# Kernel tuning notes

Measured on AMD Instinct MI355X. Metric: run time of the kernel, lower is better.

## Reference

```python
import jax, jax.numpy as jnp
import numpy as np

VOCAB, INPUT, HIDDEN = 50000, 512, 1024
BATCH, MAX_LEN = 64, 256


def setup_inputs() -> dict:
    key = jax.random.key(0)
    ks = jax.random.split(key, 16)
    s = 0.02
    return {
        "last_output": jax.random.randint(ks[0], (BATCH,), 0, VOCAB),
        "last_hidden": jax.random.normal(ks[1], (BATCH, HIDDEN), jnp.float32),
        "encoder_outputs": jax.random.normal(ks[2], (MAX_LEN, BATCH, HIDDEN), jnp.float32),
        # embedding table (padding_idx=0 just means row 0 is a pad row; math is a plain gather)
        "embedding": jax.random.uniform(ks[3], (VOCAB, INPUT), jnp.float32, -0.25, 0.25),
        # concat attention: Linear(2H -> H) and v [H]
        "attn_W": jax.random.normal(ks[4], (HIDDEN, 2 * HIDDEN), jnp.float32) * s,
        "attn_b": jnp.zeros((HIDDEN,), jnp.float32),
        "v": jax.random.normal(ks[5], (HIDDEN,), jnp.float32) * s,
        # GRU (single layer): input size = INPUT + HIDDEN, gate order r,z,n (torch order)
        "W_ih": jax.random.normal(ks[6], (3 * HIDDEN, INPUT + HIDDEN), jnp.float32) * s,
        "W_hh": jax.random.uniform(ks[7], (3 * HIDDEN, HIDDEN), jnp.float32, -0.01, 0.01),
        "b_ih": jnp.zeros((3 * HIDDEN,), jnp.float32),
        "b_hh": jnp.zeros((3 * HIDDEN,), jnp.float32),
        # output projection Linear(2H -> vocab)
        "out_W": jax.random.normal(ks[8], (VOCAB, 2 * HIDDEN), jnp.float32) * s,
        "out_b": jnp.zeros((VOCAB,), jnp.float32),
    }


def reference(last_output, last_hidden, encoder_outputs, embedding,
              attn_W, attn_b, v, W_ih, W_hh, b_ih, b_hh, out_W, out_b):
    T, B, H = encoder_outputs.shape
    # --- embedding lookup: [B, INPUT]
    emb = embedding[last_output]

    # --- concat (Bahdanau-style, no tanh in original) attention, vectorized over T
    hid = jnp.broadcast_to(last_hidden[None], (T, B, H))
    cat = jnp.concatenate([hid, encoder_outputs], axis=-1)          # [T,B,2H]
    energy = jnp.einsum('tbk,hk->tbh', cat, attn_W) + attn_b        # [T,B,H]
    scores = jnp.einsum('tbh,h->bt', energy, v)                     # [B,T]
    attn = jax.nn.softmax(scores, axis=1)                           # [B,T]

    # --- context: [B,H]
    context = jnp.einsum('bt,tbh->bh', attn, encoder_outputs)

    # --- single GRU step (torch gate order r,z,n)
    x = jnp.concatenate([emb, context], axis=-1)                    # [B, INPUT+H]
    gi = x @ W_ih.T + b_ih                                          # [B,3H]
    gh = last_hidden @ W_hh.T + b_hh                                # [B,3H]
    i_r, i_z, i_n = jnp.split(gi, 3, axis=-1)
    h_r, h_z, h_n = jnp.split(gh, 3, axis=-1)
    r = jax.nn.sigmoid(i_r + h_r)
    z = jax.nn.sigmoid(i_z + h_z)
    n = jnp.tanh(i_n + r * h_n)
    h_new = (1.0 - z) * n + z * last_hidden                         # [B,H]

    # --- output projection + log_softmax over vocab
    logits = jnp.concatenate([h_new, context], axis=-1) @ out_W.T + out_b
    logp = jax.nn.log_softmax(logits, axis=-1)                      # [B,VOCAB]
    return logp, h_new
```

## Files before the change

kernel.cpp:

```cpp
#include <hip/hip_runtime.h>
#include <cstddef>

#define VOCAB  50000
#define INPUT  512
#define HIDDEN 1024
#define BATCH  64
#define MAXLEN 256
#define NBLK   782

typedef float  f32x4 __attribute__((ext_vector_type(4)));
typedef __bf16 bf16x8 __attribute__((ext_vector_type(8)));

__device__ __forceinline__ bf16x8 cvt8(float4 a, float4 b) {
    bf16x8 r;
    r[0] = (__bf16)a.x; r[1] = (__bf16)a.y; r[2] = (__bf16)a.z; r[3] = (__bf16)a.w;
    r[4] = (__bf16)b.x; r[5] = (__bf16)b.y; r[6] = (__bf16)b.z; r[7] = (__bf16)b.w;
    return r;
}

__global__ void k_u2_part(const float* __restrict__ attn_W, const float* __restrict__ v,
                          float* __restrict__ u2p) {
    int bid = blockIdx.x, tid = threadIdx.x;
    int hq = bid >> 4, kc = bid & 15;
    int kl = tid & 63, hg = tid >> 6;
    int k = kc * 64 + kl;
    float acc = 0.f;
    int h0 = hq * 256 + hg * 64;
#pragma unroll 8
    for (int h = h0; h < h0 + 64; ++h)
        acc += v[h] * attn_W[(size_t)h * (2 * HIDDEN) + HIDDEN + k];
    __shared__ float red[4][64];
    red[hg][kl] = acc;
    __syncthreads();
    if (tid < 64)
        u2p[hq * 1024 + kc * 64 + tid] =
            red[0][tid] + red[1][tid] + red[2][tid] + red[3][tid];
}

__global__ __launch_bounds__(256) void k_att(const float* __restrict__ enc,
                                             const float* __restrict__ u2p,
                                             float* __restrict__ mpart,
                                             float* __restrict__ lpart,
                                             float* __restrict__ ctxp) {
    int bid = blockIdx.x, tid = threadIdx.x;
    int b = bid >> 2, tq = bid & 3, t0 = tq * 64;
    __shared__ float u2s[1024];
    __shared__ float s_lds[64];
    __shared__ float p_lds[64];
    for (int i = tid; i < 1024; i += 256)
        u2s[i] = u2p[i] + u2p[1024 + i] + u2p[2048 + i] + u2p[3072 + i];
    __syncthreads();
    int w = tid >> 6, lane = tid & 63;
#pragma unroll 2
    for (int it = 0; it < 16; ++it) {
        int t = t0 + w * 16 + it;
        const float* row = enc + ((size_t)t * BATCH + b) * HIDDEN;
        float acc = 0.f;
#pragma unroll
        for (int i = 0; i < 4; ++i) {
            float4 e = *(const float4*)(row + lane * 4 + i * 256);
            float4 u = *(const float4*)(&u2s[lane * 4 + i * 256]);
            acc += e.x * u.x + e.y * u.y + e.z * u.z + e.w * u.w;
        }
#pragma unroll
        for (int off = 32; off; off >>= 1) acc += __shfl_down(acc, off, 64);
        if (lane == 0) s_lds[w * 16 + it] = acc;
    }
    __syncthreads();
    float m = -INFINITY;
#pragma unroll 8
    for (int t = 0; t < 64; ++t) m = fmaxf(m, s_lds[t]);
    if (tid < 64) p_lds[tid] = expf(s_lds[tid] - m);
    __syncthreads();
    float l = 0.f;
#pragma unroll 8
    for (int t = 0; t < 64; ++t) l += p_lds[t];
    float4 acc = {0.f, 0.f, 0.f, 0.f};
    const float* ebase = enc + ((size_t)t0 * BATCH + b) * HIDDEN + tid * 4;
#pragma unroll 4
    for (int t = 0; t < 64; ++t) {
        float p = p_lds[t];
        float4 e = *(const float4*)(ebase + (size_t)t * (BATCH * HIDDEN));
        acc.x += p * e.x; acc.y += p * e.y; acc.z += p * e.z; acc.w += p * e.w;
    }
    int o = b * 4 + tq;
    *(float4*)(ctxp + (size_t)o * 1024 + tid * 4) = acc;
    if (tid == 0) { mpart[o] = m; lpart[o] = l; }
}

__global__ void k_att_comb(const float* __restrict__ mpart, const float* __restrict__ lpart,
                           const float* __restrict__ ctxp,
                           const int* __restrict__ last_output,
                           const float* __restrict__ embedding,
                           const float* __restrict__ hid,
                           __bf16* __restrict__ x_bf, __bf16* __restrict__ hid_bf,
                           __bf16* __restrict__ y_bf) {
    int b = blockIdx.x >> 2, hc = blockIdx.x & 3, tid = threadIdx.x;
    float m0 = mpart[b * 4 + 0], m1 = mpart[b * 4 + 1];
    float m2 = mpart[b * 4 + 2], m3 = mpart[b * 4 + 3];
    float M = fmaxf(fmaxf(m0, m1), fmaxf(m2, m3));
    float w0 = expf(m0 - M), w1 = expf(m1 - M), w2 = expf(m2 - M), w3 = expf(m3 - M);
    float denom = lpart[b * 4 + 0] * w0 + lpart[b * 4 + 1] * w1 +
                  lpart[b * 4 + 2] * w2 + lpart[b * 4 + 3] * w3;
    float inv = 1.f / denom;
    int h = hc * 256 + tid;
    const float* cp = ctxp + (size_t)b * 4096 + h;
    float c = (w0 * cp[0] + w1 * cp[1024] + w2 * cp[2048] + w3 * cp[3072]) * inv;
    x_bf[b * 1536 + INPUT + h]  = (__bf16)c;
    y_bf[b * 2048 + HIDDEN + h] = (__bf16)c;
    if (hc < 2)
        x_bf[b * 1536 + hc * 256 + tid] =
            (__bf16)embedding[(size_t)last_output[b] * INPUT + hc * 256 + tid];
    hid_bf[b * HIDDEN + hc * 256 + tid] = (__bf16)hid[b * HIDDEN + hc * 256 + tid];
}

__device__ __forceinline__ void gemm_tile(const float* __restrict__ W,
                                          const float* __restrict__ bias,
                                          const __bf16* __restrict__ A,
                                          float* __restrict__ out,
                                          int N, int K, int jt, int tid) {
    int wid = tid >> 6, lane = tid & 63;
    int j  = jt * 16 + (lane & 15);
    int kg = (lane >> 4) * 8;
    int kchunk = K >> 2;
    int kbeg = wid * kchunk, kend = kbeg + kchunk;
    const float*  wrow = W + (size_t)j * K;
    const __bf16* arow = A + (size_t)(lane & 15) * K;
    f32x4 acc[4] = {};
    for (int k0 = kbeg; k0 < kend; k0 += 32) {
        int kk = k0 + kg;
        float4 w0 = *(const float4*)(wrow + kk);
        float4 w1 = *(const float4*)(wrow + kk + 4);
        bf16x8 bw = cvt8(w0, w1);
#pragma unroll
        for (int mt = 0; mt < 4; ++mt) {
            bf16x8 av = *(const bf16x8*)(arow + (size_t)mt * 16 * K + kk);
            acc[mt] = __builtin_amdgcn_mfma_f32_16x16x32_bf16(av, bw, acc[mt], 0, 0, 0);
        }
    }
    __shared__ float lds[4][1024];
#pragma unroll
    for (int mt = 0; mt < 4; ++mt)
#pragma unroll
        for (int r = 0; r < 4; ++r) {
            int m = mt * 16 + (lane >> 4) * 4 + r;
            lds[wid][m * 16 + (lane & 15)] = acc[mt][r];
        }
    __syncthreads();
#pragma unroll
    for (int o = tid; o < 1024; o += 256) {
        float s = lds[0][o] + lds[1][o] + lds[2][o] + lds[3][o];
        int m = o >> 4, jl = o & 15;
        out[(size_t)m * N + jt * 16 + jl] = s + bias[jt * 16 + jl];
    }
}

__global__ __launch_bounds__(256) void k_gemm_gru(const float* __restrict__ W_ih,
                                                  const float* __restrict__ b_ih,
                                                  const __bf16* __restrict__ x_bf,
                                                  float* __restrict__ Gi,
                                                  const float* __restrict__ W_hh,
                                                  const float* __restrict__ b_hh,
                                                  const __bf16* __restrict__ hid_bf,
                                                  float* __restrict__ Gh) {
    int bid = blockIdx.x, tid = threadIdx.x;
    if (bid < 192) gemm_tile(W_ih, b_ih, x_bf,  Gi, 3072, 1536, bid,       tid);
    else           gemm_tile(W_hh, b_hh, hid_bf, Gh, 3072, 1024, bid - 192, tid);
}

__global__ void k_combine(const float* __restrict__ Gi, const float* __restrict__ Gh,
                          const float* __restrict__ hid, float* __restrict__ hnew_out,
                          __bf16* __restrict__ y_bf) {
    int idx = blockIdx.x * 256 + threadIdx.x;
    int b = idx >> 10, h = idx & 1023;
    const float* gi = Gi + (size_t)b * 3072;
    const float* gh = Gh + (size_t)b * 3072;
    float r  = 1.f / (1.f + expf(-(gi[h] + gh[h])));
    float z  = 1.f / (1.f + expf(-(gi[1024 + h] + gh[1024 + h])));
    float n  = tanhf(gi[2048 + h] + r * gh[2048 + h]);
    float hp = hid[b * HIDDEN + h];
    float hn = (1.f - z) * n + z * hp;
    hnew_out[b * HIDDEN + h] = hn;
    y_bf[b * 2048 + h] = (__bf16)hn;
}

__global__ __launch_bounds__(256) void k_gemv(const float* __restrict__ W,
                                              const float* __restrict__ bias,
                                              const __bf16* __restrict__ A,
                                              float* __restrict__ out,
                                              float* __restrict__ mw,
                                              float* __restrict__ sw) {
    int bid = blockIdx.x, tid = threadIdx.x;
    int wid = tid >> 6, lane = tid & 63;
    int kg = (lane >> 4) * 8;
    int kbeg = wid * 512;
    int ntiles = (bid == NBLK - 1) ? 1 : 4;
    int j0 = bid * 64 + (lane & 15);
    const float* wrow0 = W + (size_t)min(j0,      VOCAB - 1) * 2048;
    const float* wrow1 = W + (size_t)min(j0 + 16, VOCAB - 1) * 2048;
    const float* wrow2 = W + (size_t)min(j0 + 32, VOCAB - 1) * 2048;
    const float* wrow3 = W + (size_t)min(j0 + 48, VOCAB - 1) * 2048;
    const __bf16* arow = A + (size_t)(lane & 15) * 2048;
    f32x4 acc[4][4] = {};
    for (int k0 = kbeg; k0 < kbeg + 512; k0 += 32) {
        int kk = k0 + kg;
        bf16x8 bw0 = cvt8(*(const float4*)(wrow0 + kk), *(const float4*)(wrow0 + kk + 4));
        bf16x8 bw1 = cvt8(*(const float4*)(wrow1 + kk), *(const float4*)(wrow1 + kk + 4));
        bf16x8 bw2 = cvt8(*(const float4*)(wrow2 + kk), *(const float4*)(wrow2 + kk + 4));
        bf16x8 bw3 = cvt8(*(const float4*)(wrow3 + kk), *(const float4*)(wrow3 + kk + 4));
#pragma unroll
        for (int mt = 0; mt < 4; ++mt) {
            bf16x8 av = *(const bf16x8*)(arow + (size_t)mt * 16 * 2048 + kk);
            acc[0][mt] = __builtin_amdgcn_mfma_f32_16x16x32_bf16(av, bw0, acc[0][mt], 0, 0, 0);
            acc[1][mt] = __builtin_amdgcn_mfma_f32_16x16x32_bf16(av, bw1, acc[1][mt], 0, 0, 0);
            acc[2][mt] = __builtin_amdgcn_mfma_f32_16x16x32_bf16(av, bw2, acc[2][mt], 0, 0, 0);
            acc[3][mt] = __builtin_amdgcn_mfma_f32_16x16x32_bf16(av, bw3, acc[3][mt], 0, 0, 0);
        }
    }
    __shared__ float lds[4][1024];
    float Mreg = -INFINITY, Sreg = 0.f;
    for (int u = 0; u < ntiles; ++u) {
        if (u) __syncthreads();
#pragma unroll
        for (int mt = 0; mt < 4; ++mt)
#pragma unroll
            for (int r = 0; r < 4; ++r) {
                int m = mt * 16 + (lane >> 4) * 4 + r;
                lds[wid][m * 16 + (lane & 15)] = acc[u][mt][r];
            }
        __syncthreads();
#pragma unroll
        for (int o = tid; o < 1024; o += 256) {
            float s = lds[0][o] + lds[1][o] + lds[2][o] + lds[3][o];
            int m = o >> 4, jl = o & 15;
            int jj = bid * 64 + u * 16 + jl;
            s += bias[jj];
            out[(size_t)m * VOCAB + jj] = s;
            lds[0][o] = s;
        }
        __syncthreads();
        if (tid < 64) {
            float mx = -INFINITY;
#pragma unroll
            for (int jl = 0; jl < 16; ++jl) mx = fmaxf(mx, lds[0][tid * 16 + jl]);
            float se = 0.f;
#pragma unroll
            for (int jl = 0; jl < 16; ++jl) se += expf(lds[0][tid * 16 + jl] - mx);
            float M2 = fmaxf(Mreg, mx);
            Sreg = Sreg * expf(Mreg - M2) + se * expf(mx - M2);
            Mreg = M2;
        }
    }
    if (tid < 64) {
        mw[(size_t)tid * NBLK + bid] = Mreg;
        sw[(size_t)tid * NBLK + bid] = Sreg;
    }
}

__global__ __launch_bounds__(256) void k_lse_fused(float* __restrict__ logits,
                                                   const float* __restrict__ mw,
                                                   const float* __restrict__ sw) {
    int bid = blockIdx.x, tid = threadIdx.x;
    int b = bid / 13, c = bid % 13;
    const float* mrow = mw + (size_t)b * NBLK;
    const float* srow = sw + (size_t)b * NBLK;
    __shared__ float red[256];
    float m = -INFINITY;
    for (int i = tid; i < NBLK; i += 256) m = fmaxf(m, mrow[i]);
    red[tid] = m; __syncthreads();
    for (int off = 128; off; off >>= 1) { if (tid < off) red[tid] = fmaxf(red[tid], red[tid + off]); __syncthreads(); }
    m = red[0]; __syncthreads();
    float s = 0.f;
    for (int i = tid; i < NBLK; i += 256) s += srow[i] * expf(mrow[i] - m);
    red[tid] = s; __syncthreads();
    for (int off = 128; off; off >>= 1) { if (tid < off) red[tid] += red[tid + off]; __syncthreads(); }
    float lse = m + logf(red[0]);
    int base = c * 4096;
    int len  = min(4096, VOCAB - base);
    float* row = logits + (size_t)b * VOCAB + base;
    for (int i = tid * 4; i < len; i += 1024) {
        float4 x = *(float4*)(row + i);
        x.x -= lse; x.y -= lse; x.z -= lse; x.w -= lse;
        *(float4*)(row + i) = x;
    }
}

extern "C" void kernel_launch(void* const* d_in, const int* in_sizes, int n_in,
                              void* d_out, int out_size, void* d_ws, size_t ws_size,
                              hipStream_t stream) {
    const int*   last_output = (const int*)  d_in[0];
    const float* last_hidden = (const float*)d_in[1];
    const float* enc         = (const float*)d_in[2];
    const float* embedding   = (const float*)d_in[3];
    const float* attn_W      = (const float*)d_in[4];
    const float* v           = (const float*)d_in[6];
    const float* W_ih        = (const float*)d_in[7];
    const float* W_hh        = (const float*)d_in[8];
    const float* b_ih        = (const float*)d_in[9];
    const float* b_hh        = (const float*)d_in[10];
    const float* out_W       = (const float*)d_in[11];
    const float* out_b       = (const float*)d_in[12];

    float* out_logp = (float*)d_out;
    float* out_hnew = (float*)d_out + (size_t)BATCH * VOCAB;

    char* ws = (char*)d_ws;
    float*  u2p     = (float*) (ws + 0);
    float*  mpart   = (float*) (ws + 16384);
    float*  lpart   = (float*) (ws + 17408);
    float*  ctxp    = (float*) (ws + 18432);
    __bf16* x_bf    = (__bf16*)(ws + 1067008);
    __bf16* hid_bf  = (__bf16*)(ws + 1263616);
    __bf16* y_bf    = (__bf16*)(ws + 1394688);
    float*  Gi      = (float*) (ws + 1656832);
    float*  Gh      = (float*) (ws + 2443264);
    float*  mw      = (float*) (ws + 3229696);
    float*  sw      = (float*) (ws + 3429696);

    k_u2_part  <<<64,   256, 0, stream>>>(attn_W, v, u2p);
    k_att      <<<256,  256, 0, stream>>>(enc, u2p, mpart, lpart, ctxp);
    k_att_comb <<<256,  256, 0, stream>>>(mpart, lpart, ctxp, last_output, embedding,
                                          last_hidden, x_bf, hid_bf, y_bf);
    k_gemm_gru <<<384,  256, 0, stream>>>(W_ih, b_ih, x_bf, Gi, W_hh, b_hh, hid_bf, Gh);
    k_combine  <<<256,  256, 0, stream>>>(Gi, Gh, last_hidden, out_hnew, y_bf);
    k_gemv     <<<NBLK, 256, 0, stream>>>(out_W, out_b, y_bf, out_logp, mw, sw);
    k_lse_fused<<<832,  256, 0, stream>>>(out_logp, mw, sw);
}
```

Measured before the change: 194.4 us.

## Fuse attention combine into k_att via last-block atomic counter; move packing earlier

Removes the separate k_att_comb launch. The embedding and hidden-state bf16 packing moves into the first kernel, which runs it in extra blocks alongside the u2 reduction and also zeroes a per-batch counter. In k_att, each block increments the counter for its batch, and the last of the four blocks merges the partial softmax stats and context into x_bf and y_bf with vectorized loads. This saves a kernel launch and its dependency gap, at the cost of threadfences, an atomic per block, and serialized tail work in one block per batch.

```diff
diff --git a/kernel.cpp b/kernel.cpp
--- a/kernel.cpp
+++ b/kernel.cpp
@@ -18,35 +18,57 @@
     return r;
 }
 
-__global__ void k_u2_part(const float* __restrict__ attn_W, const float* __restrict__ v,
-                          float* __restrict__ u2p) {
-    int bid = blockIdx.x, tid = threadIdx.x;
-    int hq = bid >> 4, kc = bid & 15;
-    int kl = tid & 63, hg = tid >> 6;
-    int k = kc * 64 + kl;
-    float acc = 0.f;
-    int h0 = hq * 256 + hg * 64;
+__global__ void k_u2_pack(const float* __restrict__ attn_W, const float* __restrict__ v,
+                          float* __restrict__ u2p,
+                          const int* __restrict__ last_output,
+                          const float* __restrict__ embedding,
+                          const float* __restrict__ hid,
+                          __bf16* __restrict__ x_bf, __bf16* __restrict__ hid_bf,
+                          int* __restrict__ cnt) {
+    int bid = blockIdx.x, tid = threadIdx.x;
+    if (bid < 64) {
+        int hq = bid >> 4, kc = bid & 15;
+        int kl = tid & 63, hg = tid >> 6;
+        int k = kc * 64 + kl;
+        float acc = 0.f;
+        int h0 = hq * 256 + hg * 64;
 #pragma unroll 8
-    for (int h = h0; h < h0 + 64; ++h)
-        acc += v[h] * attn_W[(size_t)h * (2 * HIDDEN) + HIDDEN + k];
-    __shared__ float red[4][64];
-    red[hg][kl] = acc;
-    __syncthreads();
-    if (tid < 64)
-        u2p[hq * 1024 + kc * 64 + tid] =
-            red[0][tid] + red[1][tid] + red[2][tid] + red[3][tid];
+        for (int h = h0; h < h0 + 64; ++h)
+            acc += v[h] * attn_W[(size_t)h * (2 * HIDDEN) + HIDDEN + k];
+        __shared__ float red[4][64];
+        red[hg][kl] = acc;
+        __syncthreads();
+        if (tid < 64)
+            u2p[hq * 1024 + kc * 64 + tid] =
+                red[0][tid] + red[1][tid] + red[2][tid] + red[3][tid];
+    } else {
+        if (bid == 64 && tid < 64) cnt[tid] = 0;
+        int idx = (bid - 64) * 256 + tid;
+        if (idx < 64 * INPUT) {
+            int b = idx >> 9, k = idx & 511;
+            x_bf[b * 1536 + k] = (__bf16)embedding[(size_t)last_output[b] * INPUT + k];
+        } else {
+            idx -= 64 * INPUT;
+            int b = idx >> 10, h = idx & 1023;
+            hid_bf[b * HIDDEN + h] = (__bf16)hid[b * HIDDEN + h];
+        }
+    }
 }
 
 __global__ __launch_bounds__(256) void k_att(const float* __restrict__ enc,
                                              const float* __restrict__ u2p,
                                              float* __restrict__ mpart,
                                              float* __restrict__ lpart,
-                                             float* __restrict__ ctxp) {
+                                             float* __restrict__ ctxp,
+                                             int* __restrict__ cnt,
+                                             __bf16* __restrict__ x_bf,
+                                             __bf16* __restrict__ y_bf) {
     int bid = blockIdx.x, tid = threadIdx.x;
     int b = bid >> 2, tq = bid & 3, t0 = tq * 64;
     __shared__ float u2s[1024];
     __shared__ float s_lds[64];
     __shared__ float p_lds[64];
+    __shared__ int   is_last;
     for (int i = tid; i < 1024; i += 256)
         u2s[i] = u2p[i] + u2p[1024 + i] + u2p[2048 + i] + u2p[3072 + i];
     __syncthreads();
@@ -86,16 +108,11 @@
     int o = b * 4 + tq;
     *(float4*)(ctxp + (size_t)o * 1024 + tid * 4) = acc;
     if (tid == 0) { mpart[o] = m; lpart[o] = l; }
-}
-
-__global__ void k_att_comb(const float* __restrict__ mpart, const float* __restrict__ lpart,
-                           const float* __restrict__ ctxp,
-                           const int* __restrict__ last_output,
-                           const float* __restrict__ embedding,
-                           const float* __restrict__ hid,
-                           __bf16* __restrict__ x_bf, __bf16* __restrict__ hid_bf,
-                           __bf16* __restrict__ y_bf) {
-    int b = blockIdx.x >> 2, hc = blockIdx.x & 3, tid = threadIdx.x;
+    __threadfence();
+    if (tid == 0) is_last = (atomicAdd(&cnt[b], 1) == 3);
+    __syncthreads();
+    if (!is_last) return;
+    __threadfence();
     float m0 = mpart[b * 4 + 0], m1 = mpart[b * 4 + 1];
     float m2 = mpart[b * 4 + 2], m3 = mpart[b * 4 + 3];
     float M = fmaxf(fmaxf(m0, m1), fmaxf(m2, m3));
@@ -103,15 +120,20 @@
     float denom = lpart[b * 4 + 0] * w0 + lpart[b * 4 + 1] * w1 +
                   lpart[b * 4 + 2] * w2 + lpart[b * 4 + 3] * w3;
     float inv = 1.f / denom;
-    int h = hc * 256 + tid;
-    const float* cp = ctxp + (size_t)b * 4096 + h;
-    float c = (w0 * cp[0] + w1 * cp[1024] + w2 * cp[2048] + w3 * cp[3072]) * inv;
-    x_bf[b * 1536 + INPUT + h]  = (__bf16)c;
-    y_bf[b * 2048 + HIDDEN + h] = (__bf16)c;
-    if (hc < 2)
-        x_bf[b * 1536 + hc * 256 + tid] =
-            (__bf16)embedding[(size_t)last_output[b] * INPUT + hc * 256 + tid];
-    hid_bf[b * HIDDEN + hc * 256 + tid] = (__bf16)hid[b * HIDDEN + hc * 256 + tid];
+    int h4 = tid * 4;
+    const float* cp = ctxp + (size_t)b * 4096 + h4;
+    float4 c0 = *(const float4*)(cp + 0);
+    float4 c1 = *(const float4*)(cp + 1024);
+    float4 c2 = *(const float4*)(cp + 2048);
+    float4 c3 = *(const float4*)(cp + 3072);
+    float cx = (w0 * c0.x + w1 * c1.x + w2 * c2.x + w3 * c3.x) * inv;
+    float cy = (w0 * c0.y + w1 * c1.y + w2 * c2.y + w3 * c3.y) * inv;
+    float cz = (w0 * c0.z + w1 * c1.z + w2 * c2.z + w3 * c3.z) * inv;
+    float cw = (w0 * c0.w + w1 * c1.w + w2 * c2.w + w3 * c3.w) * inv;
+    __bf16* xp = x_bf + b * 1536 + INPUT + h4;
+    __bf16* yp = y_bf + b * 2048 + HIDDEN + h4;
+    xp[0] = (__bf16)cx; xp[1] = (__bf16)cy; xp[2] = (__bf16)cz; xp[3] = (__bf16)cw;
+    yp[0] = (__bf16)cx; yp[1] = (__bf16)cy; yp[2] = (__bf16)cz; yp[3] = (__bf16)cw;
 }
 
 __device__ __forceinline__ void gemm_tile(const float* __restrict__ W,
@@ -308,19 +330,19 @@
     float*  u2p     = (float*) (ws + 0);
     float*  mpart   = (float*) (ws + 16384);
     float*  lpart   = (float*) (ws + 17408);
-    float*  ctxp    = (float*) (ws + 18432);
-    __bf16* x_bf    = (__bf16*)(ws + 1067008);
-    __bf16* hid_bf  = (__bf16*)(ws + 1263616);
-    __bf16* y_bf    = (__bf16*)(ws + 1394688);
-    float*  Gi      = (float*) (ws + 1656832);
-    float*  Gh      = (float*) (ws + 2443264);
-    float*  mw      = (float*) (ws + 3229696);
-    float*  sw      = (float*) (ws + 3429696);
-
-    k_u2_part  <<<64,   256, 0, stream>>>(attn_W, v, u2p);
-    k_att      <<<256,  256, 0, stream>>>(enc, u2p, mpart, lpart, ctxp);
-    k_att_comb <<<256,  256, 0, stream>>>(mpart, lpart, ctxp, last_output, embedding,
-                                          last_hidden, x_bf, hid_bf, y_bf);
+    int*    cnt     = (int*)   (ws + 18432);
+    float*  ctxp    = (float*) (ws + 19456);
+    __bf16* x_bf    = (__bf16*)(ws + 1068032);
+    __bf16* hid_bf  = (__bf16*)(ws + 1264640);
+    __bf16* y_bf    = (__bf16*)(ws + 1395712);
+    float*  Gi      = (float*) (ws + 1657856);
+    float*  Gh      = (float*) (ws + 2444288);
+    float*  mw      = (float*) (ws + 3230720);
+    float*  sw      = (float*) (ws + 3430720);
+
+    k_u2_pack  <<<448,  256, 0, stream>>>(attn_W, v, u2p, last_output, embedding,
+                                          last_hidden, x_bf, hid_bf, cnt);
+    k_att      <<<256,  256, 0, stream>>>(enc, u2p, mpart, lpart, ctxp, cnt, x_bf, y_bf);
     k_gemm_gru <<<384,  256, 0, stream>>>(W_ih, b_ih, x_bf, Gi, W_hh, b_hh, hid_bf, Gh);
     k_combine  <<<256,  256, 0, stream>>>(Gi, Gh, last_hidden, out_hnew, y_bf);
     k_gemv     <<<NBLK, 256, 0, stream>>>(out_W, out_b, y_bf, out_logp, mw, sw);
```

Measured after the change: 232.9 us. +19.8%, slower.
